# Optimization experiments

Measured on AMD Instinct MI355X. Metric: run time of the kernel, lower is better.

## Reference

```python
import jax, jax.numpy as jnp
import numpy as np

FEAT = 512
MATCH = 256
EPS = 1e-5

def layernorm(x, gamma, beta):
    mu = jnp.mean(x, axis=-1, keepdims=True)
    var = jnp.var(x, axis=-1, keepdims=True)
    return (x - mu) * jax.lax.rsqrt(var + EPS) * gamma + beta

def setup_inputs() -> dict:
    key = jax.random.key(0)
    ks = jax.random.split(key, 5)
    B, N = 8, 2048
    patch_corr_map = jax.random.normal(ks[0], (B, N, FEAT), dtype=jnp.float32)
    W_proj = jax.random.normal(ks[1], (FEAT, MATCH), dtype=jnp.float32) * (1.0 / np.sqrt(FEAT))
    b_proj = jnp.zeros((MATCH,), dtype=jnp.float32)
    g1 = jnp.ones((MATCH,), dtype=jnp.float32)
    be1 = jnp.zeros((MATCH,), dtype=jnp.float32)
    g2 = jnp.ones((FEAT,), dtype=jnp.float32)
    be2 = jnp.zeros((FEAT,), dtype=jnp.float32)
    W_out = jax.random.normal(ks[2], (FEAT, FEAT), dtype=jnp.float32) * (1.0 / np.sqrt(FEAT))
    b_out = jnp.zeros((FEAT,), dtype=jnp.float32)
    return {"patch_corr_map": patch_corr_map, "W_proj": W_proj, "b_proj": b_proj,
            "g1": g1, "be1": be1, "g2": g2, "be2": be2, "W_out": W_out, "b_out": b_out}

def reference(patch_corr_map, W_proj, b_proj, g1, be1, g2, be2, W_out, b_out):
    # Linear feat->match, then LayerNorm; q = k = normed projection
    proj = jnp.einsum('bnf,fm->bnm', patch_corr_map, W_proj) + b_proj
    qk = layernorm(proj, g1, be1)                      # [B,N,M]
    v = layernorm(patch_corr_map, g2, be2)             # [B,N,F]
    attn = jnp.einsum('bnm,bkm->bnk', qk, qk)          # [B,N,N], no scaling (matches torch)
    attn = jax.nn.softmax(attn, axis=-1)
    out = jnp.einsum('bnk,bkf->bnf', attn, v)          # [B,N,F]
    out = out + (jnp.einsum('bnf,fg->bng', out, W_out) + b_out)
    return out
```

## Files before the change

### kernel.cpp

```cpp
#include <hip/hip_runtime.h>
#include <hip/hip_bf16.h>
#include <cstdint>
#include <cstddef>

#define FEAT 512
#define MATCH 256
#define NB 8
#define NSEQ 2048
#define NROWS (NB*NSEQ)
#define LN_EPS 1e-5f

using f32x4  = __attribute__((ext_vector_type(4))) float;
using bf16x8 = __attribute__((ext_vector_type(8))) short;
using s16x4  = __attribute__((ext_vector_type(4))) short;
using i32x4  = __attribute__((ext_vector_type(4))) int;

__device__ __forceinline__ float bf2f(short h){
  return __builtin_bit_cast(float, (uint32_t)((uint32_t)(uint16_t)h << 16));
}
__device__ __forceinline__ short f2bf(float f){
  uint32_t u = __builtin_bit_cast(uint32_t, f);
  u += 0x7FFFu + ((u >> 16) & 1u);
  return (short)(u >> 16);
}
__device__ __forceinline__ int cvtpk(float a, float b){
  int d;
  asm("v_cvt_pk_bf16_f32 %0, %1, %2" : "=v"(d) : "v"(a), "v"(b));
  return d;
}
__device__ __forceinline__ void gl_lds16(const void* g, void* l){
  __builtin_amdgcn_global_load_lds(
    (const __attribute__((address_space(1))) uint32_t*)g,
    (__attribute__((address_space(3))) uint32_t*)l, 16, 0, 0);
}
#define MFMA16(a,b,c) __builtin_amdgcn_mfma_f32_16x16x32_bf16((a),(b),(c),0,0,0)

__global__ void k_transpose_convert(const float* __restrict__ src, short* __restrict__ dst,
                                    int R, int C){
  __shared__ short tile[32][33];
  int tx = threadIdx.x, ty = threadIdx.y;
  int c0 = blockIdx.x * 32, r0 = blockIdx.y * 32;
#pragma unroll
  for (int r = 0; r < 4; r++)
    tile[ty + 8*r][tx] = f2bf(src[(size_t)(r0 + ty + 8*r) * C + c0 + tx]);
  __syncthreads();
#pragma unroll
  for (int r = 0; r < 4; r++)
    dst[(size_t)(c0 + ty + 8*r) * R + r0 + tx] = tile[tx][ty + 8*r];
}

__global__ void k_prep(const float* __restrict__ x, const float* __restrict__ g2,
                       const float* __restrict__ be2,
                       short* __restrict__ xbf, short* __restrict__ vbf){
  int w = threadIdx.x >> 6, l = threadIdx.x & 63;
  size_t row = (size_t)blockIdx.x * 4 + w;
  const float* xr = x + row * FEAT;
  float4 a = ((const float4*)xr)[l*2];
  float4 b = ((const float4*)xr)[l*2+1];
  float s  = a.x+a.y+a.z+a.w + b.x+b.y+b.z+b.w;
  float ss = a.x*a.x+a.y*a.y+a.z*a.z+a.w*a.w + b.x*b.x+b.y*b.y+b.z*b.z+b.w*b.w;
#pragma unroll
  for (int d = 1; d < 64; d <<= 1){ s += __shfl_xor(s, d); ss += __shfl_xor(ss, d); }
  float mu  = s * (1.f/FEAT);
  float var = ss * (1.f/FEAT) - mu*mu;
  float rs  = rsqrtf(var + LN_EPS);
  float4 ga = ((const float4*)g2)[l*2],  gb = ((const float4*)g2)[l*2+1];
  float4 ea = ((const float4*)be2)[l*2], eb = ((const float4*)be2)[l*2+1];
  bf16x8 xv, vv;
  float xs[8] = {a.x,a.y,a.z,a.w,b.x,b.y,b.z,b.w};
  float gs[8] = {ga.x,ga.y,ga.z,ga.w,gb.x,gb.y,gb.z,gb.w};
  float es[8] = {ea.x,ea.y,ea.z,ea.w,eb.x,eb.y,eb.z,eb.w};
#pragma unroll
  for (int i = 0; i < 8; i++){
    xv[i] = f2bf(xs[i]);
    vv[i] = f2bf((xs[i]-mu)*rs*gs[i] + es[i]);
  }
  *(bf16x8*)(xbf + row*FEAT + l*8) = xv;
  *(bf16x8*)(vbf + row*FEAT + l*8) = vv;
}

__global__ void k_ln256(const float* __restrict__ proj, const float* __restrict__ g1,
                        const float* __restrict__ be1, short* __restrict__ qkbf){
  int w = threadIdx.x >> 6, l = threadIdx.x & 63;
  size_t row = (size_t)blockIdx.x * 4 + w;
  const float* pr = proj + row * MATCH;
  float4 a = ((const float4*)pr)[l];
  float s  = a.x+a.y+a.z+a.w;
  float ss = a.x*a.x+a.y*a.y+a.z*a.z+a.w*a.w;
#pragma unroll
  for (int d = 1; d < 64; d <<= 1){ s += __shfl_xor(s, d); ss += __shfl_xor(ss, d); }
  float mu  = s * (1.f/MATCH);
  float var = ss * (1.f/MATCH) - mu*mu;
  float rs  = rsqrtf(var + LN_EPS);
  float4 g = ((const float4*)g1)[l];
  float4 e = ((const float4*)be1)[l];
  s16x4 o;
  o[0] = f2bf((a.x-mu)*rs*g.x + e.x);
  o[1] = f2bf((a.y-mu)*rs*g.y + e.y);
  o[2] = f2bf((a.z-mu)*rs*g.z + e.z);
  o[3] = f2bf((a.w-mu)*rs*g.w + e.w);
  *(s16x4*)(qkbf + row*MATCH + l*4) = o;
}

__global__ void k_transpose_v(const short* __restrict__ src, short* __restrict__ dst){
  __shared__ short tile[32][33];
  int tx = threadIdx.x, ty = threadIdx.y;
  int bz = blockIdx.z;
  int n0 = blockIdx.x * 32, f0 = blockIdx.y * 32;
  const short* s = src + (size_t)bz * NSEQ * FEAT;
  short*       d = dst + (size_t)bz * FEAT * NSEQ;
#pragma unroll
  for (int r = 0; r < 4; r++)
    tile[ty + 8*r][tx] = s[(size_t)(n0 + ty + 8*r) * FEAT + f0 + tx];
  __syncthreads();
#pragma unroll
  for (int r = 0; r < 4; r++)
    d[(size_t)(f0 + ty + 8*r) * NSEQ + n0 + tx] = tile[tx][ty + 8*r];
}

template<int MODE>
__global__ void k_gemm(const short* __restrict__ A, const short* __restrict__ BT,
                       const float* __restrict__ bias, const short* __restrict__ addbf,
                       float* __restrict__ C, int Kdim, int Ncols){
  __shared__ __align__(16) short lA[128*64];
  __shared__ __align__(16) short lB[128*64];
  int t = threadIdx.x, l = t & 63, w = t >> 6;
  int mq = w & 1, nq = w >> 1;
  int m0 = blockIdx.x * 128, n0 = blockIdx.y * 128;
  f32x4 acc[4][4] = {};
  for (int k0 = 0; k0 < Kdim; k0 += 64){
#pragma unroll
    for (int it = 0; it < 4; it++){
      int c = w*4 + it;
      gl_lds16(A  + (size_t)(m0 + 8*c + (l>>3))*Kdim + k0 + (l&7)*8, (char*)lA + c*1024);
      gl_lds16(BT + (size_t)(n0 + 8*c + (l>>3))*Kdim + k0 + (l&7)*8, (char*)lB + c*1024);
    }
    __syncthreads();
#pragma unroll
    for (int ks = 0; ks < 2; ks++){
      bf16x8 af[4], bfr[4];
#pragma unroll
      for (int i = 0; i < 4; i++)
        af[i]  = *(const bf16x8*)&lA[(64*mq + 16*i + (l&15))*64 + ks*32 + (l>>4)*8];
#pragma unroll
      for (int j = 0; j < 4; j++)
        bfr[j] = *(const bf16x8*)&lB[(64*nq + 16*j + (l&15))*64 + ks*32 + (l>>4)*8];
#pragma unroll
      for (int i = 0; i < 4; i++)
#pragma unroll
        for (int j = 0; j < 4; j++)
          acc[i][j] = MFMA16(af[i], bfr[j], acc[i][j]);
    }
    __syncthreads();
  }
#pragma unroll
  for (int i = 0; i < 4; i++)
#pragma unroll
    for (int j = 0; j < 4; j++){
      int col = n0 + 64*nq + 16*j + (l&15);
      float bv = bias[col];
#pragma unroll
      for (int r = 0; r < 4; r++){
        int row = m0 + 64*mq + 16*i + ((l>>4)<<2) + r;
        float v = acc[i][j][r] + bv;
        if (MODE == 1) v += bf2f(addbf[(size_t)row*Ncols + col]);
        C[(size_t)row*Ncols + col] = v;
      }
    }
}

#define KVB5 64
#define NT5  (NSEQ/KVB5)

__device__ __forceinline__ void stage_K5(const char* qkb, int kv0, char* lKb, int w, int l){
#pragma unroll
  for (int i = 0; i < 4; i++){
    int c = w*4 + i;
    int row = 2*c + (l>>5);
    int col = ((l&31)*16) ^ ((row&15)<<4);
    gl_lds16(qkb + (size_t)(kv0+row)*512 + col, lKb + c*1024);
  }
}
__device__ __forceinline__ void stage_V5(const char* vTb, int kv0, char* lVb, int w, int l){
#pragma unroll
  for (int i = 0; i < 8; i++){
    int c = w*8 + i;
    int row = 8*c + (l>>3);
    int col = ((l&7)*16) ^ ((row&7)<<4);
    gl_lds16(vTb + (size_t)row*4096 + (size_t)kv0*2 + col, lVb + c*1024);
  }
}

__launch_bounds__(512)
__global__ void k_attn5(const short* __restrict__ qk, const short* __restrict__ vT,
                        short* __restrict__ obf){
  __shared__ __align__(16) char lds[140544];
  char*  Vb   = lds + 65536;
  char*  Pb   = lds + 131072;
  float* denL = (float*)(lds + 139264);
  float* invL = (float*)(lds + 140288);
  int tdx = threadIdx.x, l = tdx & 63, w = tdx >> 6;
  int g = l >> 4, q = l & 15;
  int b  = blockIdx.x & 7;
  int q0 = (blockIdx.x >> 3) * 64;
  int kvf = w & 3, qfp = w >> 2;
  int fq  = w;
  const char* qkb = (const char*)(qk + (size_t)b * NSEQ * MATCH);
  const char* vTb = (const char*)(vT + (size_t)b * FEAT * NSEQ);
  bf16x8 qfr[2][8];
#pragma unroll
  for (int j = 0; j < 2; j++){
    const char* qr = qkb + (size_t)(q0 + 16*(2*qfp+j) + q)*512 + g*16;
#pragma unroll
    for (int ks = 0; ks < 8; ks++) qfr[j][ks] = *(const bf16x8*)(qr + ks*64);
  }
  f32x4 accO[4][4] = {};
  float den0 = 0.f, den1 = 0.f;
  int pkq = (q & 7) << 4;

  stage_K5(qkb, 0, lds, w, l);
  stage_V5(vTb, 0, Vb, w, l);
  __syncthreads();
  for (int tt = 0; tt < NT5; tt++){
    const char* Kcur = lds + ((tt&1) ? 32768 : 0);
    char*       Knxt = lds + ((tt&1) ? 0 : 32768);
    if (tt)           stage_V5(vTb, tt*KVB5, Vb, w, l);
    if (tt + 1 < NT5) stage_K5(qkb, (tt+1)*KVB5, Knxt, w, l);
    f32x4 s0 = {}, s1 = {};
    const char* krow = Kcur + (size_t)(16*kvf + q)*512;
#pragma unroll
    for (int ks = 0; ks < 8; ks++){
      bf16x8 kf = *(const bf16x8*)(krow + ((ks*64 + 16*g) ^ (q<<4)));
      s0 = MFMA16(kf, qfr[0][ks], s0);
      s1 = MFMA16(kf, qfr[1][ks], s1);
    }
    float p0[4], p1[4];
#pragma unroll
    for (int r = 0; r < 4; r++){ p0[r] = __expf(s0[r] - 256.0f);
                                 p1[r] = __expf(s1[r] - 256.0f); }
    den0 += (p0[0]+p0[1]) + (p0[2]+p0[3]);
    den1 += (p1[0]+p1[1]) + (p1[2]+p1[3]);
    {
      int2 w0; w0.x = cvtpk(p0[0], p0[1]); w0.y = cvtpk(p0[2], p0[3]);
      int2 w1; w1.x = cvtpk(p1[0], p1[1]); w1.y = cvtpk(p1[2], p1[3]);
      int qg0 = 32*qfp + q, qg1 = qg0 + 16;
      int kb  = 32*kvf + 8*g;
      *(int2*)(Pb + qg0*128 + (kb ^ pkq)) = w0;
      *(int2*)(Pb + qg1*128 + (kb ^ pkq)) = w1;
    }
    __syncthreads();
    __builtin_amdgcn_s_setprio(1);
#pragma unroll
    for (int st = 0; st < 2; st++){
      bf16x8 pa[4];
      int kvb = (64*st + 16*g) ^ pkq;
#pragma unroll
      for (int qf = 0; qf < 4; qf++)
        pa[qf] = *(const bf16x8*)(Pb + (16*qf + q)*128 + kvb);
#pragma unroll
      for (int fn = 0; fn < 4; fn++){
        int frow = 64*fq + 16*fn + q;
        bf16x8 vf = *(const bf16x8*)(Vb + (size_t)frow*128 + ((64*st + 16*g) ^ pkq));
#pragma unroll
        for (int qf = 0; qf < 4; qf++)
          accO[qf][fn] = MFMA16(pa[qf], vf, accO[qf][fn]);
      }
    }
    __builtin_amdgcn_s_setprio(0);
    __syncthreads();
  }
  den0 += __shfl_xor(den0, 16); den0 += __shfl_xor(den0, 32);
  den1 += __shfl_xor(den1, 16); den1 += __shfl_xor(den1, 32);
  if (g == 0){
    denL[(kvf*4 + 2*qfp    )*16 + q] = den0;
    denL[(kvf*4 + 2*qfp + 1)*16 + q] = den1;
  }
  __syncthreads();
  if (w == 0){
    float s = denL[(0*4 + (l>>4))*16 + (l&15)] + denL[(1*4 + (l>>4))*16 + (l&15)]
            + denL[(2*4 + (l>>4))*16 + (l&15)] + denL[(3*4 + (l>>4))*16 + (l&15)];
    invL[l] = 1.0f / s;
  }
  __syncthreads();
  float invr[4][4];
#pragma unroll
  for (int qf = 0; qf < 4; qf++)
#pragma unroll
    for (int rr = 0; rr < 4; rr++)
      invr[qf][rr] = invL[16*qf + 4*g + rr];
#pragma unroll
  for (int qf = 0; qf < 4; qf++)
#pragma unroll
    for (int fn = 0; fn < 4; fn++)
#pragma unroll
      for (int rr = 0; rr < 4; rr++){
        int row = q0 + 16*qf + 4*g + rr;
        int col = 64*fq + 16*fn + q;
        obf[((size_t)b * NSEQ + row) * FEAT + col] = f2bf(accO[qf][fn][rr] * invr[qf][rr]);
      }
}

extern "C" void kernel_launch(void* const* d_in, const int* in_sizes, int n_in,
                              void* d_out, int out_size, void* d_ws, size_t ws_size,
                              hipStream_t stream) {
  const float* x   = (const float*)d_in[0];
  const float* Wp  = (const float*)d_in[1];
  const float* bp  = (const float*)d_in[2];
  const float* g1  = (const float*)d_in[3];
  const float* be1 = (const float*)d_in[4];
  const float* g2  = (const float*)d_in[5];
  const float* be2 = (const float*)d_in[6];
  const float* Wo  = (const float*)d_in[7];
  const float* bo  = (const float*)d_in[8];
  float* out = (float*)d_out;

  char* ws = (char*)d_ws;
  short* xbf  = (short*)ws;
  short* vT   = xbf;
  short* vbf  = (short*)(ws + 16777216);
  short* qkbf = (short*)(ws + 33554432);
  float* proj = (float*)(ws + 41943040);
  short* obf  = (short*)(ws + 41943040);
  short* WpT  = (short*)(ws + 58720256);
  short* WoT  = (short*)(ws + 58982400);

  dim3 tb(32, 8, 1);
  k_transpose_convert<<<dim3(MATCH/32, FEAT/32, 1), tb, 0, stream>>>(Wp, WpT, FEAT, MATCH);
  k_transpose_convert<<<dim3(FEAT/32,  FEAT/32, 1), tb, 0, stream>>>(Wo, WoT, FEAT, FEAT);
  k_prep<<<NROWS/4, 256, 0, stream>>>(x, g2, be2, xbf, vbf);
  k_gemm<0><<<dim3(NROWS/128, MATCH/128, 1), 256, 0, stream>>>(xbf, WpT, bp, nullptr, proj, FEAT, MATCH);
  k_ln256<<<NROWS/4, 256, 0, stream>>>(proj, g1, be1, qkbf);
  k_transpose_v<<<dim3(NSEQ/32, FEAT/32, NB), tb, 0, stream>>>(vbf, vT);
  k_attn5<<<NB * (NSEQ/64), 512, 0, stream>>>(qkbf, vT, obf);
  k_gemm<1><<<dim3(NROWS/128, FEAT/128, 1), 256, 0, stream>>>(obf, WoT, bo, obf, out, FEAT, FEAT);
}
```

Measured before the change: 137.8 us.

## Fuse projection GEMM with LayerNorm and register-buffer V in attention

Replaces the projection GEMM plus separate LayerNorm kernel with one kernel. It computes a 64x256 output tile per block and reduces row statistics across waves in LDS, which removes the fp32 proj write/read round trip and one launch. The attention kernel now loads V fragments straight from global memory into double-buffered registers instead of staging them in LDS. The loop is unrolled by two with explicit waitcnt and barriers, which cuts LDS use from about 140KB to 75KB and may allow more occupancy. The last iteration prefetches K and V past the end of the sequence; those loads stay inside the workspace but fetch unused data, and register pressure goes up.

```diff
diff --git a/kernel.cpp b/kernel.cpp
--- a/kernel.cpp
+++ b/kernel.cpp
@@ -79,29 +79,6 @@
   *(bf16x8*)(vbf + row*FEAT + l*8) = vv;
 }
 
-__global__ void k_ln256(const float* __restrict__ proj, const float* __restrict__ g1,
-                        const float* __restrict__ be1, short* __restrict__ qkbf){
-  int w = threadIdx.x >> 6, l = threadIdx.x & 63;
-  size_t row = (size_t)blockIdx.x * 4 + w;
-  const float* pr = proj + row * MATCH;
-  float4 a = ((const float4*)pr)[l];
-  float s  = a.x+a.y+a.z+a.w;
-  float ss = a.x*a.x+a.y*a.y+a.z*a.z+a.w*a.w;
-#pragma unroll
-  for (int d = 1; d < 64; d <<= 1){ s += __shfl_xor(s, d); ss += __shfl_xor(ss, d); }
-  float mu  = s * (1.f/MATCH);
-  float var = ss * (1.f/MATCH) - mu*mu;
-  float rs  = rsqrtf(var + LN_EPS);
-  float4 g = ((const float4*)g1)[l];
-  float4 e = ((const float4*)be1)[l];
-  s16x4 o;
-  o[0] = f2bf((a.x-mu)*rs*g.x + e.x);
-  o[1] = f2bf((a.y-mu)*rs*g.y + e.y);
-  o[2] = f2bf((a.z-mu)*rs*g.z + e.z);
-  o[3] = f2bf((a.w-mu)*rs*g.w + e.w);
-  *(s16x4*)(qkbf + row*MATCH + l*4) = o;
-}
-
 __global__ void k_transpose_v(const short* __restrict__ src, short* __restrict__ dst){
   __shared__ short tile[32][33];
   int tx = threadIdx.x, ty = threadIdx.y;
@@ -116,6 +93,90 @@
 #pragma unroll
   for (int r = 0; r < 4; r++)
     d[(size_t)(f0 + ty + 8*r) * NSEQ + n0 + tx] = tile[tx][ty + 8*r];
+}
+
+__global__ void k_gemm_ln(const short* __restrict__ A, const short* __restrict__ BT,
+                          const float* __restrict__ bias, const float* __restrict__ g1,
+                          const float* __restrict__ be1, short* __restrict__ qkbf){
+  __shared__ __align__(16) short lA[64*64];
+  __shared__ __align__(16) short lB[256*64];
+  __shared__ float red[2][64][2];
+  int t = threadIdx.x, l = t & 63, w = t >> 6;
+  int mq = w & 1, nq = w >> 1;
+  int m0 = blockIdx.x * 64;
+  f32x4 acc[2][8] = {};
+  for (int k0 = 0; k0 < FEAT; k0 += 64){
+#pragma unroll
+    for (int i = 0; i < 2; i++){
+      int c = w*2 + i;
+      gl_lds16(A + (size_t)(m0 + 8*c + (l>>3))*FEAT + k0 + (l&7)*8, (char*)lA + c*1024);
+    }
+#pragma unroll
+    for (int i = 0; i < 8; i++){
+      int c = w*8 + i;
+      gl_lds16(BT + (size_t)(8*c + (l>>3))*FEAT + k0 + (l&7)*8, (char*)lB + c*1024);
+    }
+    __syncthreads();
+#pragma unroll
+    for (int ks = 0; ks < 2; ks++){
+      bf16x8 af[2], bfr[8];
+#pragma unroll
+      for (int i = 0; i < 2; i++)
+        af[i] = *(const bf16x8*)&lA[(32*mq + 16*i + (l&15))*64 + ks*32 + (l>>4)*8];
+#pragma unroll
+      for (int j = 0; j < 8; j++)
+        bfr[j] = *(const bf16x8*)&lB[(128*nq + 16*j + (l&15))*64 + ks*32 + (l>>4)*8];
+#pragma unroll
+      for (int i = 0; i < 2; i++)
+#pragma unroll
+        for (int j = 0; j < 8; j++)
+          acc[i][j] = MFMA16(af[i], bfr[j], acc[i][j]);
+    }
+    __syncthreads();
+  }
+  float g1v[8], bev[8];
+#pragma unroll
+  for (int j = 0; j < 8; j++){
+    int col = 128*nq + 16*j + (l&15);
+    float bv = bias[col];
+#pragma unroll
+    for (int i = 0; i < 2; i++)
+#pragma unroll
+      for (int r = 0; r < 4; r++) acc[i][j][r] += bv;
+    g1v[j] = g1[col]; bev[j] = be1[col];
+  }
+#pragma unroll
+  for (int i = 0; i < 2; i++)
+#pragma unroll
+    for (int r = 0; r < 4; r++){
+      float s = 0.f, ss = 0.f;
+#pragma unroll
+      for (int j = 0; j < 8; j++){ float c = acc[i][j][r]; s += c; ss += c*c; }
+#pragma unroll
+      for (int d = 1; d < 16; d <<= 1){ s += __shfl_xor(s, d); ss += __shfl_xor(ss, d); }
+      if ((l & 15) == 0){
+        int rowL = 32*mq + 16*i + 4*(l>>4) + r;
+        red[nq][rowL][0] = s; red[nq][rowL][1] = ss;
+      }
+    }
+  __syncthreads();
+#pragma unroll
+  for (int i = 0; i < 2; i++)
+#pragma unroll
+    for (int r = 0; r < 4; r++){
+      int rowL = 32*mq + 16*i + 4*(l>>4) + r;
+      float s  = red[0][rowL][0] + red[1][rowL][0];
+      float ss = red[0][rowL][1] + red[1][rowL][1];
+      float mu = s * (1.f/MATCH);
+      float var = ss * (1.f/MATCH) - mu*mu;
+      float rs = rsqrtf(var + LN_EPS);
+      size_t rowg = (size_t)(m0 + rowL) * MATCH;
+#pragma unroll
+      for (int j = 0; j < 8; j++){
+        int col = 128*nq + 16*j + (l&15);
+        qkbf[rowg + col] = f2bf((acc[i][j][r] - mu)*rs*g1v[j] + bev[j]);
+      }
+    }
 }
 
 template<int MODE>
@@ -181,93 +242,102 @@
     gl_lds16(qkb + (size_t)(kv0+row)*512 + col, lKb + c*1024);
   }
 }
-__device__ __forceinline__ void stage_V5(const char* vTb, int kv0, char* lVb, int w, int l){
-#pragma unroll
-  for (int i = 0; i < 8; i++){
-    int c = w*8 + i;
-    int row = 8*c + (l>>3);
-    int col = ((l&7)*16) ^ ((row&7)<<4);
-    gl_lds16(vTb + (size_t)row*4096 + (size_t)kv0*2 + col, lVb + c*1024);
-  }
-}
+
+#define ATTN_BODY(TT, KCUR, KNXT, VCUR, VNXT)                                        \
+  {                                                                                  \
+    stage_K5(qkb, ((TT)+1)*KVB5, (char*)(KNXT), w, l);                               \
+    {                                                                                \
+      int kv0 = ((TT)+1)*KVB5;                                                       \
+      _Pragma("unroll")                                                              \
+      for (int st = 0; st < 2; st++)                                                 \
+        _Pragma("unroll")                                                            \
+        for (int fn = 0; fn < 4; fn++)                                               \
+          VNXT[st*4+fn] = *(const bf16x8*)(vTb                                       \
+              + (size_t)(64*w + 16*fn + q)*4096 + (size_t)(kv0 + 32*st + 8*g)*2);    \
+    }                                                                                \
+    __builtin_amdgcn_sched_barrier(0);                                               \
+    f32x4 s0 = {}, s1 = {};                                                          \
+    const char* krow = (const char*)(KCUR) + (size_t)(16*kvf + q)*512;               \
+    _Pragma("unroll")                                                                \
+    for (int ks = 0; ks < 8; ks++){                                                  \
+      bf16x8 kf = *(const bf16x8*)(krow + ((ks*64 + 16*g) ^ (q<<4)));                \
+      s0 = MFMA16(kf, qfr0[ks], s0);                                                 \
+      s1 = MFMA16(kf, qfr1[ks], s1);                                                 \
+    }                                                                                \
+    float p0[4], p1[4];                                                              \
+    _Pragma("unroll")                                                                \
+    for (int r = 0; r < 4; r++){ p0[r] = __expf(s0[r] - 256.0f);                     \
+                                 p1[r] = __expf(s1[r] - 256.0f); }                   \
+    den0 += (p0[0]+p0[1]) + (p0[2]+p0[3]);                                           \
+    den1 += (p1[0]+p1[1]) + (p1[2]+p1[3]);                                           \
+    {                                                                                \
+      int2 w0; w0.x = cvtpk(p0[0], p0[1]); w0.y = cvtpk(p0[2], p0[3]);               \
+      int2 w1; w1.x = cvtpk(p1[0], p1[1]); w1.y = cvtpk(p1[2], p1[3]);               \
+      int qg0 = 32*qfp + q;                                                          \
+      int kb  = 32*kvf + 8*g;                                                        \
+      *(int2*)(Pb + qg0*128 + (kb ^ pkq)) = w0;                                      \
+      *(int2*)(Pb + (qg0+16)*128 + (kb ^ pkq)) = w1;                                 \
+    }                                                                                \
+    asm volatile("s_waitcnt lgkmcnt(0)" ::: "memory");                               \
+    __builtin_amdgcn_s_barrier();                                                    \
+    __builtin_amdgcn_s_setprio(1);                                                   \
+    _Pragma("unroll")                                                                \
+    for (int st = 0; st < 2; st++){                                                  \
+      bf16x8 pa[4];                                                                  \
+      int kvb = (64*st + 16*g) ^ pkq;                                                \
+      _Pragma("unroll")                                                              \
+      for (int qf = 0; qf < 4; qf++)                                                 \
+        pa[qf] = *(const bf16x8*)(Pb + (16*qf + q)*128 + kvb);                       \
+      _Pragma("unroll")                                                              \
+      for (int fn = 0; fn < 4; fn++)                                                 \
+        _Pragma("unroll")                                                            \
+        for (int qf = 0; qf < 4; qf++)                                               \
+          accO[qf][fn] = MFMA16(pa[qf], VCUR[st*4+fn], accO[qf][fn]);                \
+    }                                                                                \
+    __builtin_amdgcn_s_setprio(0);                                                   \
+    asm volatile("s_waitcnt vmcnt(8) lgkmcnt(0)" ::: "memory");                      \
+    __builtin_amdgcn_s_barrier();                                                    \
+  }
 
 __launch_bounds__(512)
-__global__ void k_attn5(const short* __restrict__ qk, const short* __restrict__ vT,
+__global__ void k_attn8(const short* __restrict__ qk, const short* __restrict__ vT,
                         short* __restrict__ obf){
-  __shared__ __align__(16) char lds[140544];
-  char*  Vb   = lds + 65536;
-  char*  Pb   = lds + 131072;
-  float* denL = (float*)(lds + 139264);
-  float* invL = (float*)(lds + 140288);
+  __shared__ __align__(16) char lds[75008];
+  char*  Pb   = lds + 65536;
+  float* denL = (float*)(lds + 73728);
+  float* invL = (float*)(lds + 74752);
   int tdx = threadIdx.x, l = tdx & 63, w = tdx >> 6;
   int g = l >> 4, q = l & 15;
   int b  = blockIdx.x & 7;
   int q0 = (blockIdx.x >> 3) * 64;
   int kvf = w & 3, qfp = w >> 2;
-  int fq  = w;
   const char* qkb = (const char*)(qk + (size_t)b * NSEQ * MATCH);
   const char* vTb = (const char*)(vT + (size_t)b * FEAT * NSEQ);
-  bf16x8 qfr[2][8];
-#pragma unroll
-  for (int j = 0; j < 2; j++){
-    const char* qr = qkb + (size_t)(q0 + 16*(2*qfp+j) + q)*512 + g*16;
-#pragma unroll
-    for (int ks = 0; ks < 8; ks++) qfr[j][ks] = *(const bf16x8*)(qr + ks*64);
+  bf16x8 qfr0[8], qfr1[8];
+  {
+    const char* qr0 = qkb + (size_t)(q0 + 16*(2*qfp) + q)*512 + g*16;
+    const char* qr1 = qr0 + 16*512;
+#pragma unroll
+    for (int ks = 0; ks < 8; ks++){ qfr0[ks] = *(const bf16x8*)(qr0 + ks*64);
+                                    qfr1[ks] = *(const bf16x8*)(qr1 + ks*64); }
   }
   f32x4 accO[4][4] = {};
   float den0 = 0.f, den1 = 0.f;
   int pkq = (q & 7) << 4;
+  bf16x8 vA[8], vB[8];
 
   stage_K5(qkb, 0, lds, w, l);
-  stage_V5(vTb, 0, Vb, w, l);
-  __syncthreads();
-  for (int tt = 0; tt < NT5; tt++){
-    const char* Kcur = lds + ((tt&1) ? 32768 : 0);
-    char*       Knxt = lds + ((tt&1) ? 0 : 32768);
-    if (tt)           stage_V5(vTb, tt*KVB5, Vb, w, l);
-    if (tt + 1 < NT5) stage_K5(qkb, (tt+1)*KVB5, Knxt, w, l);
-    f32x4 s0 = {}, s1 = {};
-    const char* krow = Kcur + (size_t)(16*kvf + q)*512;
-#pragma unroll
-    for (int ks = 0; ks < 8; ks++){
-      bf16x8 kf = *(const bf16x8*)(krow + ((ks*64 + 16*g) ^ (q<<4)));
-      s0 = MFMA16(kf, qfr[0][ks], s0);
-      s1 = MFMA16(kf, qfr[1][ks], s1);
-    }
-    float p0[4], p1[4];
-#pragma unroll
-    for (int r = 0; r < 4; r++){ p0[r] = __expf(s0[r] - 256.0f);
-                                 p1[r] = __expf(s1[r] - 256.0f); }
-    den0 += (p0[0]+p0[1]) + (p0[2]+p0[3]);
-    den1 += (p1[0]+p1[1]) + (p1[2]+p1[3]);
-    {
-      int2 w0; w0.x = cvtpk(p0[0], p0[1]); w0.y = cvtpk(p0[2], p0[3]);
-      int2 w1; w1.x = cvtpk(p1[0], p1[1]); w1.y = cvtpk(p1[2], p1[3]);
-      int qg0 = 32*qfp + q, qg1 = qg0 + 16;
-      int kb  = 32*kvf + 8*g;
-      *(int2*)(Pb + qg0*128 + (kb ^ pkq)) = w0;
-      *(int2*)(Pb + qg1*128 + (kb ^ pkq)) = w1;
-    }
-    __syncthreads();
-    __builtin_amdgcn_s_setprio(1);
-#pragma unroll
-    for (int st = 0; st < 2; st++){
-      bf16x8 pa[4];
-      int kvb = (64*st + 16*g) ^ pkq;
-#pragma unroll
-      for (int qf = 0; qf < 4; qf++)
-        pa[qf] = *(const bf16x8*)(Pb + (16*qf + q)*128 + kvb);
-#pragma unroll
-      for (int fn = 0; fn < 4; fn++){
-        int frow = 64*fq + 16*fn + q;
-        bf16x8 vf = *(const bf16x8*)(Vb + (size_t)frow*128 + ((64*st + 16*g) ^ pkq));
-#pragma unroll
-        for (int qf = 0; qf < 4; qf++)
-          accO[qf][fn] = MFMA16(pa[qf], vf, accO[qf][fn]);
-      }
-    }
-    __builtin_amdgcn_s_setprio(0);
-    __syncthreads();
+#pragma unroll
+  for (int st = 0; st < 2; st++)
+#pragma unroll
+    for (int fn = 0; fn < 4; fn++)
+      vA[st*4+fn] = *(const bf16x8*)(vTb
+          + (size_t)(64*w + 16*fn + q)*4096 + (size_t)(32*st + 8*g)*2);
+  asm volatile("s_waitcnt vmcnt(8)" ::: "memory");
+  __builtin_amdgcn_s_barrier();
+  for (int tt = 0; tt < NT5; tt += 2){
+    ATTN_BODY(tt,   lds,         lds + 32768, vA, vB)
+    ATTN_BODY(tt+1, lds + 32768, lds,         vB, vA)
   }
   den0 += __shfl_xor(den0, 16); den0 += __shfl_xor(den0, 32);
   den1 += __shfl_xor(den1, 16); den1 += __shfl_xor(den1, 32);
@@ -295,7 +365,7 @@
 #pragma unroll
       for (int rr = 0; rr < 4; rr++){
         int row = q0 + 16*qf + 4*g + rr;
-        int col = 64*fq + 16*fn + q;
+        int col = 64*w + 16*fn + q;
         obf[((size_t)b * NSEQ + row) * FEAT + col] = f2bf(accO[qf][fn][rr] * invr[qf][rr]);
       }
 }
@@ -319,7 +389,6 @@
   short* vT   = xbf;
   short* vbf  = (short*)(ws + 16777216);
   short* qkbf = (short*)(ws + 33554432);
-  float* proj = (float*)(ws + 41943040);
   short* obf  = (short*)(ws + 41943040);
   short* WpT  = (short*)(ws + 58720256);
   short* WoT  = (short*)(ws + 58982400);
@@ -328,9 +397,8 @@
   k_transpose_convert<<<dim3(MATCH/32, FEAT/32, 1), tb, 0, stream>>>(Wp, WpT, FEAT, MATCH);
   k_transpose_convert<<<dim3(FEAT/32,  FEAT/32, 1), tb, 0, stream>>>(Wo, WoT, FEAT, FEAT);
   k_prep<<<NROWS/4, 256, 0, stream>>>(x, g2, be2, xbf, vbf);
-  k_gemm<0><<<dim3(NROWS/128, MATCH/128, 1), 256, 0, stream>>>(xbf, WpT, bp, nullptr, proj, FEAT, MATCH);
-  k_ln256<<<NROWS/4, 256, 0, stream>>>(proj, g1, be1, qkbf);
+  k_gemm_ln<<<NROWS/64, 256, 0, stream>>>(xbf, WpT, bp, g1, be1, qkbf);
   k_transpose_v<<<dim3(NSEQ/32, FEAT/32, NB), tb, 0, stream>>>(vbf, vT);
-  k_attn5<<<NB * (NSEQ/64), 512, 0, stream>>>(qkbf, vT, obf);
+  k_attn8<<<NB * (NSEQ/64), 512, 0, stream>>>(qkbf, vT, obf);
   k_gemm<1><<<dim3(NROWS/128, FEAT/128, 1), 256, 0, stream>>>(obf, WoT, bo, obf, out, FEAT, FEAT);
 }
```

Result: slower. 173.7 us (+26.0%).
